# Optimization experiments

Measured on AMD Instinct MI355X. Metric: run time of the kernel, lower is better.

Reference implementation:

```python
import jax, jax.numpy as jnp
import numpy as np

WIN = 7          # window height/width
P = 10           # prompts_len
HEADS = 12
B0 = 32          # image batch (spa_prompts batch)
NW = 64          # windows per image
NW_TOK = WIN * WIN  # 49


def _relative_position_index(w):
    coords = np.stack(np.meshgrid(np.arange(w), np.arange(w), indexing='ij'))  # [2,w,w]
    flat = coords.reshape(2, -1)                        # [2, w*w]
    rel = flat[:, :, None] - flat[:, None, :]           # [2, w*w, w*w]
    rel = rel.transpose(1, 2, 0).astype(np.int64)       # [w*w, w*w, 2]
    rel[..., 0] += w - 1
    rel[..., 1] += w - 1
    rel[..., 0] *= 2 * w - 1
    return rel.sum(-1)                                  # [w*w, w*w]

REL_IDX = jnp.asarray(_relative_position_index(WIN))    # [49,49] int


def setup_inputs() -> dict:
    key = jax.random.key(0)
    ks = jax.random.split(key, 8)
    dim = 384
    return {
        'x': jax.random.normal(ks[0], (B0 * NW, NW_TOK, dim), jnp.float32),
        'spa_prompts': jax.random.normal(ks[1], (B0, P, dim), jnp.float32),
        'mask': jax.random.normal(ks[2], (NW, NW_TOK, NW_TOK), jnp.float32),
        'bias_table': jax.random.normal(ks[3], (169, HEADS), jnp.float32) * 0.02,
        'w_qkv': jax.random.normal(ks[4], (3 * dim, dim), jnp.float32) * 0.02,
        'b_qkv': jax.random.normal(ks[5], (3 * dim,), jnp.float32) * 0.02,
        'w_proj': jax.random.normal(ks[6], (dim, dim), jnp.float32) * 0.02,
        'b_proj': jax.random.normal(ks[7], (dim,), jnp.float32) * 0.02,
    }


def reference(x, spa_prompts, mask, bias_table, w_qkv, b_qkv, w_proj, b_proj):
    B_, Nw, C = x.shape
    b0 = spa_prompts.shape[0]
    nW = B_ // b0
    hd = C // HEADS
    scale = hd ** -0.5

    # broadcast prompts to every window and prepend
    prompts = jnp.broadcast_to(spa_prompts[:, None], (b0, nW, P, C)).reshape(B_, P, C)
    xc = jnp.concatenate([prompts, x], axis=1)          # [B_, N, C], N = P + Nw
    N = xc.shape[1]

    qkv = xc @ w_qkv.T + b_qkv                          # [B_, N, 3C]
    qkv = qkv.reshape(B_, N, 3, HEADS, hd).transpose(2, 0, 3, 1, 4)
    q, k, v = qkv[0], qkv[1], qkv[2]                    # [B_, H, N, hd]

    attn_weight = jnp.einsum('bhnd,bhmd->bhnm', q, k)   # unscaled, returned

    # relative position bias gathered for the window block, padded over prompt rows/cols
    rpb = bias_table[REL_IDX.reshape(-1)].reshape(NW_TOK, NW_TOK, HEADS)
    rpb = rpb.transpose(2, 0, 1)                        # [H, 49, 49]
    bias_full = jnp.pad(rpb, ((0, 0), (P, 0), (P, 0)))  # [H, N, N]

    attn = attn_weight * scale + bias_full[None]

    mask_full = jnp.pad(mask, ((0, 0), (P, 0), (P, 0)))  # [nW, N, N]
    attn = attn.reshape(b0, nW, HEADS, N, N) + mask_full[None, :, None]
    attn = jax.nn.softmax(attn.reshape(B_, HEADS, N, N), axis=-1)

    out = jnp.einsum('bhnm,bhmd->bnhd', attn, v).reshape(B_, N, C)
    out = out @ w_proj.T + b_proj

    prompts_out = out[:, :P].reshape(b0, nW, P, C).mean(axis=1)
    x_out = out[:, P:]
    return (x_out, attn_weight, prompts_out)
```

## Files before the change

kernel.cpp:

```cpp
#include <hip/hip_runtime.h>
#include <hip/hip_bf16.h>

#define P     10
#define NTOK  59
#define HEADS 12
#define NWTOK 49

#define AW_OFF 38535168
#define PO_OFF 124096512

typedef __attribute__((ext_vector_type(8))) short short8;
typedef __attribute__((ext_vector_type(8))) unsigned short ushort8;
typedef __attribute__((ext_vector_type(4))) float floatx4;
typedef float f4u __attribute__((ext_vector_type(4), aligned(4)));
typedef unsigned int uint_g __attribute__((address_space(1)));
typedef unsigned int uint_l __attribute__((address_space(3)));

__device__ __forceinline__ unsigned short f2b(float f) {
  unsigned u = __builtin_bit_cast(unsigned, f);
  u += 0x7fffu + ((u >> 16) & 1u);
  return (unsigned short)(u >> 16);
}

__device__ __forceinline__ void gll16(const void* g, void* l) {
  __builtin_amdgcn_global_load_lds((const uint_g*)g, (uint_l*)l, 16, 0, 0);
}

__device__ __forceinline__ int xcd_swz(int bid, int nwg) {
  const int q = nwg >> 3, r = nwg & 7;
  const int xcd = bid & 7, ord = bid >> 3;
  return (xcd < r ? xcd * (q + 1) : r * (q + 1) + (xcd - r) * q) + ord;
}

__global__ __launch_bounds__(256) void convert_w_kernel(
    const float* __restrict__ w, unsigned short* __restrict__ wb) {
  const int i = (blockIdx.x * 256 + threadIdx.x) * 8;
  const float4 a = *(const float4*)(w + i);
  const float4 b = *(const float4*)(w + i + 4);
  ushort8 o;
  o[0] = f2b(a.x); o[1] = f2b(a.y); o[2] = f2b(a.z); o[3] = f2b(a.w);
  o[4] = f2b(b.x); o[5] = f2b(b.y); o[6] = f2b(b.z); o[7] = f2b(b.w);
  *(ushort8*)(wb + i) = o;
}

__global__ __launch_bounds__(256) void combo_kernel(
    const float* __restrict__ mask, const float* __restrict__ bias_table,
    float* __restrict__ combo) {
  const int bid = blockIdx.x;
  const int h = bid % HEADS, wnd = bid / HEADS;
#pragma unroll
  for (int e0 = 0; e0 < 4096; e0 += 256) {
    const int e = e0 + threadIdx.x;
    const int ti = e >> 6, tj = e & 63;
    float v = 0.f;
    if (ti >= P && ti < NTOK && tj >= P && tj < NTOK) {
      const int a = ti - P, c = tj - P;
      const int ai = a / 7, aj = a - ai * 7;
      const int bi = c / 7, bj = c - bi * 7;
      const int ridx = (ai - bi + 6) * 13 + (aj - bj + 6);
      v = bias_table[ridx * HEADS + h] + mask[((size_t)wnd * 49 + a) * 49 + c];
    }
    combo[((size_t)bid << 12) + e] = v;
  }
}

__global__ __launch_bounds__(256) void gemm_qkv_kernel(
    const unsigned short* __restrict__ xb, const unsigned short* __restrict__ xp,
    const unsigned short* __restrict__ Bw, const float* __restrict__ b_qkv,
    unsigned short* __restrict__ qkx, unsigned short* __restrict__ qkp) {
  __shared__ unsigned short sbuf[18432];
  unsigned short* Asw = sbuf;
  unsigned short* Bsw = sbuf + 8192;
  const int t = threadIdx.x;
  const int w = t >> 6, lane = t & 63;
  const int lr = lane & 15, lg = lane >> 4;
  const int w0 = w >> 1, w1 = w & 1;
  const int wg = xcd_swz(blockIdx.x, 9 * 787);
  const int cb = wg % 9;
  const int my = wg / 9;
  const bool isP = my >= 784;
  const int n0 = cb * 128;
  const int srow = lane >> 3, cpos = lane & 7;

  floatx4 acc[4][4];
#pragma unroll
  for (int mr = 0; mr < 4; ++mr)
#pragma unroll
    for (int nc = 0; nc < 4; ++nc) acc[mr][nc] = (floatx4)0.f;

  for (int k0 = 0; k0 < 384; k0 += 64) {
#pragma unroll
    for (int i = 0; i < 4; ++i) {
      const int r = (w * 4 + i) * 8 + srow;
      const int c = cpos ^ (r & 7);
      const unsigned short* asrc;
      if (!isP) {
        asrc = xb + (size_t)(my * 128 + r) * 384 + k0 + c * 8;
      } else {
        int mp = (my - 784) * 128 + r;
        if (mp > 319) mp = 319;
        asrc = xp + (size_t)mp * 384 + k0 + c * 8;
      }
      gll16(asrc, Asw + (w * 4 + i) * 512);
      gll16(Bw + (size_t)(n0 + r) * 384 + k0 + c * 8, Bsw + (w * 4 + i) * 512);
    }
    __syncthreads();
#pragma unroll
    for (int kh = 0; kh < 2; ++kh) {
      short8 af[4], bf[4];
#pragma unroll
      for (int mr = 0; mr < 4; ++mr) {
        const int r = w0 * 64 + mr * 16 + lr;
        af[mr] = *(const short8*)(Asw + r * 64 + (((kh * 4 + lg) ^ (r & 7)) * 8));
      }
#pragma unroll
      for (int nc = 0; nc < 4; ++nc) {
        const int r = w1 * 64 + nc * 16 + lr;
        bf[nc] = *(const short8*)(Bsw + r * 64 + (((kh * 4 + lg) ^ (r & 7)) * 8));
      }
#pragma unroll
      for (int mr = 0; mr < 4; ++mr)
#pragma unroll
        for (int nc = 0; nc < 4; ++nc)
          acc[mr][nc] = __builtin_amdgcn_mfma_f32_16x16x32_bf16(
              af[mr], bf[nc], acc[mr][nc], 0, 0, 0);
    }
    __syncthreads();
  }

  const int sec = cb / 3;
  const int nis = (cb - sec * 3) * 128;
  float bias[4];
#pragma unroll
  for (int nc = 0; nc < 4; ++nc)
    bias[nc] = b_qkv[n0 + w1 * 64 + nc * 16 + lr];

  unsigned short* rp = sbuf + w * 4608;
#pragma unroll
  for (int mr = 0; mr < 4; ++mr)
#pragma unroll
    for (int nc = 0; nc < 4; ++nc)
#pragma unroll
      for (int reg = 0; reg < 4; ++reg)
        rp[(mr * 16 + lg * 4 + reg) * 72 + nc * 16 + lr] =
            f2b(acc[mr][nc][reg] + bias[nc]);
  __syncthreads();

  const int rr = lane;
  unsigned short* dst = nullptr;
  if (!isP) {
    const int m = my * 128 + w0 * 64 + rr;
    const int bb = m / 49, tok = m - bb * 49;
    dst = qkx + ((size_t)(bb * 3 + sec) * 49 + tok) * 384 + nis + w1 * 64;
  } else {
    const int mp = (my - 784) * 128 + w0 * 64 + rr;
    if (mp < 320) {
      const int b0 = mp / 10, ptok = mp - b0 * 10;
      dst = qkp + ((size_t)(b0 * 3 + sec) * 10 + ptok) * 384 + nis + w1 * 64;
    }
  }
  if (dst) {
#pragma unroll
    for (int u = 0; u < 8; ++u)
      *(ushort8*)(dst + u * 8) = *(const ushort8*)(rp + rr * 72 + u * 8);
  }
}

__global__ __launch_bounds__(256) void attn_kernel(
    const unsigned short* __restrict__ qkx, const unsigned short* __restrict__ qkp,
    const float* __restrict__ combo, float* __restrict__ aw_out,
    unsigned short* __restrict__ attn_bf) {
  __shared__ char lds[14976];
  unsigned short* qs = (unsigned short*)(lds);
  unsigned short* ks = (unsigned short*)(lds + 5120);
  unsigned short* vt = (unsigned short*)(lds + 10240);
  unsigned short* Pm = (unsigned short*)(lds);

  const int blk = blockIdx.x;
  const int b = blk / HEADS, h = blk - b * HEADS;
  const int t = threadIdx.x;
  const int w = t >> 6, lane = t & 63, lr = lane & 15, lg = lane >> 4;

  if (t < 236) {
    const int row = t >> 2, dc = (t & 3) * 8;
    ushort8 q8, k8, v8;
    if (row < P) {
      const unsigned short* pb =
          qkp + ((size_t)((b >> 6) * 3) * 10 + row) * 384 + h * 32 + dc;
      q8 = *(const ushort8*)(pb);
      k8 = *(const ushort8*)(pb + 10 * 384);
      v8 = *(const ushort8*)(pb + 20 * 384);
    } else {
      const unsigned short* xbp =
          qkx + ((size_t)(b * 3) * 49 + (row - P)) * 384 + h * 32 + dc;
      q8 = *(const ushort8*)(xbp);
      k8 = *(const ushort8*)(xbp + 49 * 384);
      v8 = *(const ushort8*)(xbp + 98 * 384);
    }
    *(ushort8*)(qs + row * 40 + dc) = q8;
    *(ushort8*)(ks + row * 40 + dc) = k8;
#pragma unroll
    for (int j = 0; j < 8; ++j) vt[(dc + j) * 74 + row] = v8[j];
  } else {
    const int e = t - 236;
#pragma unroll
    for (int jj = 0; jj < 8; ++jj) {
      const int f = e * 8 + jj;
      vt[(f / 5) * 74 + 59 + (f % 5)] = 0;
    }
  }
  __syncthreads();

  const int q = w * 16 + lr;
  const short8 qa = *(const short8*)(qs + q * 40 + lg * 8);
  floatx4 sacc[4];
#pragma unroll
  for (int nt = 0; nt < 4; ++nt) {
    const short8 kb = *(const short8*)(ks + (nt * 16 + lr) * 40 + lg * 8);
    sacc[nt] = __builtin_amdgcn_mfma_f32_16x16x32_bf16(kb, qa, (floatx4)0.f, 0, 0, 0);
  }

  if (q < NTOK) {
    float* rowp = aw_out + (size_t)blk * 3481 + q * 59;
#pragma unroll
    for (int nt = 0; nt < 3; ++nt)
      *(f4u*)(rowp + nt * 16 + lg * 4) = __builtin_bit_cast(f4u, sacc[nt]);
    if (lg < 2) {
      *(f4u*)(rowp + 48 + lg * 4) = __builtin_bit_cast(f4u, sacc[3]);
    } else if (lg == 2) {
      rowp[56] = sacc[3][0];
      rowp[57] = sacc[3][1];
      rowp[58] = sacc[3][2];
    }
  }

  const float scale = 0.17677669529663687f;
  const float* comb = combo + (((size_t)((b & 63) * HEADS + h)) << 12) + q * 64;
  float ev[4][4];
  float mx = -3.0e38f;
#pragma unroll
  for (int nt = 0; nt < 4; ++nt) {
    const float4 c4 = *(const float4*)(comb + nt * 16 + lg * 4);
    const float cc[4] = {c4.x, c4.y, c4.z, c4.w};
#pragma unroll
    for (int reg = 0; reg < 4; ++reg) {
      const int kk2 = nt * 16 + lg * 4 + reg;
      const float v = (q < NTOK && kk2 < NTOK)
                          ? fmaf(sacc[nt][reg], scale, cc[reg])
                          : -3.0e38f;
      ev[nt][reg] = v;
      mx = fmaxf(mx, v);
    }
  }
  mx = fmaxf(mx, __shfl_xor(mx, 16));
  mx = fmaxf(mx, __shfl_xor(mx, 32));
  float sm = 0.f;
#pragma unroll
  for (int nt = 0; nt < 4; ++nt)
#pragma unroll
    for (int reg = 0; reg < 4; ++reg) {
      const float e = __expf(ev[nt][reg] - mx);
      ev[nt][reg] = e;
      sm += e;
    }
  sm += __shfl_xor(sm, 16);
  sm += __shfl_xor(sm, 32);
  const float inv = 1.0f / sm;

  __syncthreads();
#pragma unroll
  for (int nt = 0; nt < 4; ++nt) {
    uint2 uu;
    uu.x = (unsigned)f2b(ev[nt][0] * inv) | ((unsigned)f2b(ev[nt][1] * inv) << 16);
    uu.y = (unsigned)f2b(ev[nt][2] * inv) | ((unsigned)f2b(ev[nt][3] * inv) << 16);
    *(uint2*)(Pm + q * 72 + nt * 16 + lg * 4) = uu;
  }

  floatx4 oacc[2];
  oacc[0] = (floatx4)0.f; oacc[1] = (floatx4)0.f;
#pragma unroll
  for (int kk = 0; kk < 2; ++kk) {
    const short8 pa = *(const short8*)(Pm + (w * 16 + lr) * 72 + kk * 32 + lg * 8);
#pragma unroll
    for (int nt = 0; nt < 2; ++nt) {
      const short8 vb = *(const short8*)(vt + (nt * 16 + lr) * 74 + kk * 32 + lg * 8);
      oacc[nt] = __builtin_amdgcn_mfma_f32_16x16x32_bf16(pa, vb, oacc[nt], 0, 0, 0);
    }
  }

  unsigned short* wb = Pm + w * 1152;
#pragma unroll
  for (int nt = 0; nt < 2; ++nt)
#pragma unroll
    for (int reg = 0; reg < 4; ++reg)
      wb[(lg * 4 + reg) * 40 + nt * 16 + lr] = f2b(oacc[nt][reg]);
  const int rr = lane >> 2, c8 = (lane & 3) * 8;
  const int row = w * 16 + rr;
  if (row < NTOK) {
    const ushort8 ov = *(const ushort8*)(wb + rr * 40 + c8);
    *(ushort8*)(attn_bf + ((size_t)(b * NTOK + row)) * 384 + h * 32 + c8) = ov;
  }
}

__global__ __launch_bounds__(256) void gemm_proj_kernel(
    const unsigned short* __restrict__ A, const unsigned short* __restrict__ Bw,
    const float* __restrict__ b_proj, float* __restrict__ x_out,
    float* __restrict__ pbuf) {
  __shared__ unsigned short Asw[8192];
  __shared__ unsigned short Bsw[8192];
  const int t = threadIdx.x;
  const int w = t >> 6, lane = t & 63;
  const int lr = lane & 15, lg = lane >> 4;
  const int w0 = w >> 1, w1 = w & 1;
  const int wg = xcd_swz(blockIdx.x, 3 * 944);
  const size_t m0 = (size_t)(wg / 3) * 128;
  const int n0 = (wg % 3) * 128;
  const int srow = lane >> 3, cpos = lane & 7;

  floatx4 acc[4][4];
#pragma unroll
  for (int mr = 0; mr < 4; ++mr)
#pragma unroll
    for (int nc = 0; nc < 4; ++nc) acc[mr][nc] = (floatx4)0.f;

  for (int k0 = 0; k0 < 384; k0 += 64) {
#pragma unroll
    for (int i = 0; i < 4; ++i) {
      const int r = (w * 4 + i) * 8 + srow;
      const int c = cpos ^ (r & 7);
      gll16(A + (m0 + r) * 384 + k0 + c * 8, Asw + (w * 4 + i) * 512);
      gll16(Bw + (size_t)(n0 + r) * 384 + k0 + c * 8, Bsw + (w * 4 + i) * 512);
    }
    __syncthreads();
#pragma unroll
    for (int kh = 0; kh < 2; ++kh) {
      short8 af[4], bf[4];
#pragma unroll
      for (int mr = 0; mr < 4; ++mr) {
        const int r = w0 * 64 + mr * 16 + lr;
        af[mr] = *(const short8*)(Asw + r * 64 + (((kh * 4 + lg) ^ (r & 7)) * 8));
      }
#pragma unroll
      for (int nc = 0; nc < 4; ++nc) {
        const int r = w1 * 64 + nc * 16 + lr;
        bf[nc] = *(const short8*)(Bsw + r * 64 + (((kh * 4 + lg) ^ (r & 7)) * 8));
      }
#pragma unroll
      for (int mr = 0; mr < 4; ++mr)
#pragma unroll
        for (int nc = 0; nc < 4; ++nc)
          acc[mr][nc] = __builtin_amdgcn_mfma_f32_16x16x32_bf16(
              af[mr], bf[nc], acc[mr][nc], 0, 0, 0);
    }
    __syncthreads();
  }

  float bias[4]; int nn[4];
#pragma unroll
  for (int nc = 0; nc < 4; ++nc) {
    nn[nc] = n0 + w1 * 64 + nc * 16 + lr;
    bias[nc] = b_proj[nn[nc]];
  }
#pragma unroll
  for (int mr = 0; mr < 4; ++mr)
#pragma unroll
    for (int reg = 0; reg < 4; ++reg) {
      const int m = (int)m0 + w0 * 64 + mr * 16 + lg * 4 + reg;
      const int bb = m / 59, tok = m - bb * 59;
      float* dst = (tok >= P)
          ? x_out + (size_t)(bb * NWTOK + tok - P) * 384
          : pbuf + (size_t)(bb * P + tok) * 384;
#pragma unroll
      for (int nc = 0; nc < 4; ++nc)
        dst[nn[nc]] = acc[mr][nc][reg] + bias[nc];
    }
}

__global__ __launch_bounds__(256) void reduce_prompts_kernel(
    const float* __restrict__ pbuf, float* __restrict__ po) {
  const int o = blockIdx.x * 256 + threadIdx.x;
  const int b0 = o / 3840;
  const int rem = o - b0 * 3840;
  const float* base = pbuf + (size_t)b0 * 64 * 3840 + rem;
  float s = 0.f;
#pragma unroll 8
  for (int w = 0; w < 64; ++w) s += base[(size_t)w * 3840];
  po[o] = s * (1.f / 64.f);
}

extern "C" void kernel_launch(void* const* d_in, const int* in_sizes, int n_in,
                              void* d_out, int out_size, void* d_ws, size_t ws_size,
                              hipStream_t stream) {
  const float* x          = (const float*)d_in[0];
  const float* spa        = (const float*)d_in[1];
  const float* mask       = (const float*)d_in[2];
  const float* bias_table = (const float*)d_in[3];
  const float* w_qkv      = (const float*)d_in[4];
  const float* b_qkv      = (const float*)d_in[5];
  const float* w_proj     = (const float*)d_in[6];
  const float* b_proj     = (const float*)d_in[7];
  float* out = (float*)d_out;

  unsigned short* x_bf     = (unsigned short*)d_ws;
  unsigned short* attn_bf  = (unsigned short*)d_ws;
  unsigned short* xp_bf    = (unsigned short*)((char*)d_ws + 77070336ULL);
  unsigned short* wqkv_bf  = (unsigned short*)((char*)d_ws + 77316096ULL);
  unsigned short* qkx      = (unsigned short*)((char*)d_ws + 92798976ULL);
  unsigned short* qkp      = (unsigned short*)((char*)d_ws + 324009984ULL);
  unsigned short* wproj_bf = (unsigned short*)((char*)d_ws + 324747264ULL);
  float*          pbuf     = (float*)((char*)d_ws + 325042176ULL);
  float*          combo    = (float*)((char*)d_ws + 356499456ULL);

  convert_w_kernel<<<18816, 256, 0, stream>>>(x, x_bf);
  convert_w_kernel<<<60, 256, 0, stream>>>(spa, xp_bf);
  convert_w_kernel<<<216, 256, 0, stream>>>(w_qkv, wqkv_bf);
  convert_w_kernel<<<72, 256, 0, stream>>>(w_proj, wproj_bf);
  combo_kernel<<<768, 256, 0, stream>>>(mask, bias_table, combo);
  gemm_qkv_kernel<<<9 * 787, 256, 0, stream>>>(x_bf, xp_bf, wqkv_bf, b_qkv,
                                               qkx, qkp);
  attn_kernel<<<2048 * HEADS, 256, 0, stream>>>(qkx, qkp, combo, out + AW_OFF,
                                                attn_bf);
  gemm_proj_kernel<<<3 * 944, 256, 0, stream>>>(attn_bf, wproj_bf, b_proj,
                                                out, pbuf);
  reduce_prompts_kernel<<<480, 256, 0, stream>>>(pbuf, out + PO_OFF);
}
```

Before: 596.4 us.

## Fuse fp32-to-bf16 conversion of activations into QKV GEMM A-tile loads

Removes the separate conversion kernels for x and the prompts. The QKV GEMM now reads fp32 activations directly, converts them to bf16 in registers and writes them to swizzled LDS, instead of loading a pre-converted bf16 copy through direct global-to-LDS loads. This saves writing and re-reading a large bf16 copy of x. In exchange, each GEMM tile reads twice the bytes and the A loads go through registers, and x is re-read by all 9 column blocks. The attention kernel's block index is also remapped with the XCD swizzle to improve cache locality across dies.

```diff
diff --git a/kernel.cpp b/kernel.cpp
--- a/kernel.cpp
+++ b/kernel.cpp
@@ -65,7 +65,7 @@
 }
 
 __global__ __launch_bounds__(256) void gemm_qkv_kernel(
-    const unsigned short* __restrict__ xb, const unsigned short* __restrict__ xp,
+    const float* __restrict__ x, const float* __restrict__ spa,
     const unsigned short* __restrict__ Bw, const float* __restrict__ b_qkv,
     unsigned short* __restrict__ qkx, unsigned short* __restrict__ qkp) {
   __shared__ unsigned short sbuf[18432];
@@ -89,20 +89,36 @@
     for (int nc = 0; nc < 4; ++nc) acc[mr][nc] = (floatx4)0.f;
 
   for (int k0 = 0; k0 < 384; k0 += 64) {
+    ushort8 av[4];
 #pragma unroll
     for (int i = 0; i < 4; ++i) {
       const int r = (w * 4 + i) * 8 + srow;
       const int c = cpos ^ (r & 7);
-      const unsigned short* asrc;
+      const float* asrc;
       if (!isP) {
-        asrc = xb + (size_t)(my * 128 + r) * 384 + k0 + c * 8;
+        asrc = x + (size_t)(my * 128 + r) * 384 + k0 + c * 8;
       } else {
         int mp = (my - 784) * 128 + r;
         if (mp > 319) mp = 319;
-        asrc = xp + (size_t)mp * 384 + k0 + c * 8;
+        asrc = spa + (size_t)mp * 384 + k0 + c * 8;
       }
-      gll16(asrc, Asw + (w * 4 + i) * 512);
+      const float4 v0 = ((const float4*)asrc)[0];
+      const float4 v1 = ((const float4*)asrc)[1];
+      ushort8 o;
+      o[0] = f2b(v0.x); o[1] = f2b(v0.y); o[2] = f2b(v0.z); o[3] = f2b(v0.w);
+      o[4] = f2b(v1.x); o[5] = f2b(v1.y); o[6] = f2b(v1.z); o[7] = f2b(v1.w);
+      av[i] = o;
+    }
+#pragma unroll
+    for (int i = 0; i < 4; ++i) {
+      const int r = (w * 4 + i) * 8 + srow;
+      const int c = cpos ^ (r & 7);
       gll16(Bw + (size_t)(n0 + r) * 384 + k0 + c * 8, Bsw + (w * 4 + i) * 512);
+    }
+#pragma unroll
+    for (int i = 0; i < 4; ++i) {
+      const int r = (w * 4 + i) * 8 + srow;
+      *(ushort8*)(Asw + r * 64 + cpos * 8) = av[i];
     }
     __syncthreads();
 #pragma unroll
@@ -176,7 +192,7 @@
   unsigned short* vt = (unsigned short*)(lds + 10240);
   unsigned short* Pm = (unsigned short*)(lds);
 
-  const int blk = blockIdx.x;
+  const int blk = xcd_swz(blockIdx.x, 2048 * HEADS);
   const int b = blk / HEADS, h = blk - b * HEADS;
   const int t = threadIdx.x;
   const int w = t >> 6, lane = t & 63, lr = lane & 15, lg = lane >> 4;
@@ -401,9 +417,7 @@
   const float* b_proj     = (const float*)d_in[7];
   float* out = (float*)d_out;
 
-  unsigned short* x_bf     = (unsigned short*)d_ws;
   unsigned short* attn_bf  = (unsigned short*)d_ws;
-  unsigned short* xp_bf    = (unsigned short*)((char*)d_ws + 77070336ULL);
   unsigned short* wqkv_bf  = (unsigned short*)((char*)d_ws + 77316096ULL);
   unsigned short* qkx      = (unsigned short*)((char*)d_ws + 92798976ULL);
   unsigned short* qkp      = (unsigned short*)((char*)d_ws + 324009984ULL);
@@ -411,12 +425,10 @@
   float*          pbuf     = (float*)((char*)d_ws + 325042176ULL);
   float*          combo    = (float*)((char*)d_ws + 356499456ULL);
 
-  convert_w_kernel<<<18816, 256, 0, stream>>>(x, x_bf);
-  convert_w_kernel<<<60, 256, 0, stream>>>(spa, xp_bf);
   convert_w_kernel<<<216, 256, 0, stream>>>(w_qkv, wqkv_bf);
   convert_w_kernel<<<72, 256, 0, stream>>>(w_proj, wproj_bf);
   combo_kernel<<<768, 256, 0, stream>>>(mask, bias_table, combo);
-  gemm_qkv_kernel<<<9 * 787, 256, 0, stream>>>(x_bf, xp_bf, wqkv_bf, b_qkv,
+  gemm_qkv_kernel<<<9 * 787, 256, 0, stream>>>(x, spa, wqkv_bf, b_qkv,
                                                qkx, qkp);
   attn_kernel<<<2048 * HEADS, 256, 0, stream>>>(qkx, qkp, combo, out + AW_OFF,
                                                 attn_bf);
```

New measurement: 605.0 us. About the same (+1.4%).

## Fuse window attention with output projection in one per-window kernel

Applied to the files above, without the earlier changes.

Replaces the per-(window,head) attention kernel and the separate projection GEMM with one kernel per window. It loops over all 12 heads, keeps the bf16 attention output for the window in LDS, then multiplies it by w_proj directly. The P matrix now moves between lanes with shuffles instead of a trip through LDS. This removes the global round trip of the attention intermediate and one launch. In exchange it uses about 73KB of LDS per block, which lowers occupancy, runs only 2048 blocks, and reloads w_proj from L2 for every window.

```diff
diff --git a/kernel.cpp b/kernel.cpp
--- a/kernel.cpp
+++ b/kernel.cpp
@@ -166,214 +166,196 @@
   }
 }
 
-__global__ __launch_bounds__(256) void attn_kernel(
+__global__ __launch_bounds__(256) void attn_proj_kernel(
     const unsigned short* __restrict__ qkx, const unsigned short* __restrict__ qkp,
-    const float* __restrict__ combo, float* __restrict__ aw_out,
-    unsigned short* __restrict__ attn_bf) {
-  __shared__ char lds[14976];
-  unsigned short* qs = (unsigned short*)(lds);
-  unsigned short* ks = (unsigned short*)(lds + 5120);
-  unsigned short* vt = (unsigned short*)(lds + 10240);
-  unsigned short* Pm = (unsigned short*)(lds);
-
-  const int blk = blockIdx.x;
-  const int b = blk / HEADS, h = blk - b * HEADS;
+    const float* __restrict__ combo, const unsigned short* __restrict__ wproj,
+    const float* __restrict__ b_proj, float* __restrict__ aw_out,
+    float* __restrict__ x_out, float* __restrict__ pbuf) {
+  __shared__ char lds[74752];
+  unsigned short* Obuf = (unsigned short*)lds;
+  unsigned short* qs   = (unsigned short*)(lds + 50176);
+  unsigned short* ks   = (unsigned short*)(lds + 55296);
+  unsigned short* vt   = (unsigned short*)(lds + 60416);
+  unsigned short* Bst  = (unsigned short*)(lds + 50176);
+
+  const int b = blockIdx.x;
   const int t = threadIdx.x;
   const int w = t >> 6, lane = t & 63, lr = lane & 15, lg = lane >> 4;
-
-  if (t < 236) {
-    const int row = t >> 2, dc = (t & 3) * 8;
-    ushort8 q8, k8, v8;
-    if (row < P) {
-      const unsigned short* pb =
-          qkp + ((size_t)((b >> 6) * 3) * 10 + row) * 384 + h * 32 + dc;
-      q8 = *(const ushort8*)(pb);
-      k8 = *(const ushort8*)(pb + 10 * 384);
-      v8 = *(const ushort8*)(pb + 20 * 384);
+  const float scale = 0.17677669529663687f;
+  const int q = w * 16 + lr;
+
+  for (int h = 0; h < HEADS; ++h) {
+    __syncthreads();
+    if (t < 236) {
+      const int row = t >> 2, dc = (t & 3) * 8;
+      ushort8 q8, k8, v8;
+      if (row < P) {
+        const unsigned short* pb =
+            qkp + ((size_t)((b >> 6) * 3) * 10 + row) * 384 + h * 32 + dc;
+        q8 = *(const ushort8*)(pb);
+        k8 = *(const ushort8*)(pb + 10 * 384);
+        v8 = *(const ushort8*)(pb + 20 * 384);
+      } else {
+        const unsigned short* xbp =
+            qkx + ((size_t)(b * 3) * 49 + (row - P)) * 384 + h * 32 + dc;
+        q8 = *(const ushort8*)(xbp);
+        k8 = *(const ushort8*)(xbp + 49 * 384);
+        v8 = *(const ushort8*)(xbp + 98 * 384);
+      }
+      *(ushort8*)(qs + row * 40 + dc) = q8;
+      *(ushort8*)(ks + row * 40 + dc) = k8;
+#pragma unroll
+      for (int j = 0; j < 8; ++j) vt[(dc + j) * 74 + row] = v8[j];
     } else {
-      const unsigned short* xbp =
-          qkx + ((size_t)(b * 3) * 49 + (row - P)) * 384 + h * 32 + dc;
-      q8 = *(const ushort8*)(xbp);
-      k8 = *(const ushort8*)(xbp + 49 * 384);
-      v8 = *(const ushort8*)(xbp + 98 * 384);
-    }
-    *(ushort8*)(qs + row * 40 + dc) = q8;
-    *(ushort8*)(ks + row * 40 + dc) = k8;
-#pragma unroll
-    for (int j = 0; j < 8; ++j) vt[(dc + j) * 74 + row] = v8[j];
-  } else {
-    const int e = t - 236;
-#pragma unroll
-    for (int jj = 0; jj < 8; ++jj) {
-      const int f = e * 8 + jj;
-      vt[(f / 5) * 74 + 59 + (f % 5)] = 0;
-    }
+      const int e = t - 236;
+#pragma unroll
+      for (int jj = 0; jj < 8; ++jj) {
+        const int f = e * 8 + jj;
+        vt[(f / 5) * 74 + 59 + (f % 5)] = 0;
+      }
+    }
+    __syncthreads();
+
+    const short8 qa = *(const short8*)(qs + q * 40 + lg * 8);
+    floatx4 sacc[4];
+#pragma unroll
+    for (int nt = 0; nt < 4; ++nt) {
+      const short8 kb = *(const short8*)(ks + (nt * 16 + lr) * 40 + lg * 8);
+      sacc[nt] =
+          __builtin_amdgcn_mfma_f32_16x16x32_bf16(kb, qa, (floatx4)0.f, 0, 0, 0);
+    }
+
+    if (q < NTOK) {
+      float* rowp = aw_out + ((size_t)(b * HEADS + h)) * 3481 + q * 59;
+#pragma unroll
+      for (int nt = 0; nt < 3; ++nt)
+        *(f4u*)(rowp + nt * 16 + lg * 4) = __builtin_bit_cast(f4u, sacc[nt]);
+      if (lg < 2) {
+        *(f4u*)(rowp + 48 + lg * 4) = __builtin_bit_cast(f4u, sacc[3]);
+      } else if (lg == 2) {
+        rowp[56] = sacc[3][0]; rowp[57] = sacc[3][1]; rowp[58] = sacc[3][2];
+      }
+    }
+
+    const float* comb =
+        combo + (((size_t)((b & 63) * HEADS + h)) << 12) + q * 64;
+    float ev[4][4];
+    float mx = -3.0e38f;
+#pragma unroll
+    for (int nt = 0; nt < 4; ++nt) {
+      const float4 c4 = *(const float4*)(comb + nt * 16 + lg * 4);
+      const float cc[4] = {c4.x, c4.y, c4.z, c4.w};
+#pragma unroll
+      for (int reg = 0; reg < 4; ++reg) {
+        const int kk2 = nt * 16 + lg * 4 + reg;
+        const float v = (q < NTOK && kk2 < NTOK)
+                            ? fmaf(sacc[nt][reg], scale, cc[reg])
+                            : -3.0e38f;
+        ev[nt][reg] = v;
+        mx = fmaxf(mx, v);
+      }
+    }
+    mx = fmaxf(mx, __shfl_xor(mx, 16));
+    mx = fmaxf(mx, __shfl_xor(mx, 32));
+    float sm = 0.f;
+#pragma unroll
+    for (int nt = 0; nt < 4; ++nt)
+#pragma unroll
+      for (int reg = 0; reg < 4; ++reg) {
+        const float e = __expf(ev[nt][reg] - mx);
+        ev[nt][reg] = e;
+        sm += e;
+      }
+    sm += __shfl_xor(sm, 16);
+    sm += __shfl_xor(sm, 32);
+    const float inv = 1.0f / sm;
+
+    unsigned pk[4][2];
+#pragma unroll
+    for (int nt = 0; nt < 4; ++nt)
+#pragma unroll
+      for (int pp = 0; pp < 2; ++pp)
+        pk[nt][pp] = (unsigned)f2b(ev[nt][2 * pp] * inv) |
+                     ((unsigned)f2b(ev[nt][2 * pp + 1] * inv) << 16);
+
+    floatx4 oacc[2];
+    oacc[0] = (floatx4)0.f; oacc[1] = (floatx4)0.f;
+#pragma unroll
+    for (int kk = 0; kk < 2; ++kk) {
+      unsigned W4[4];
+#pragma unroll
+      for (int jp = 0; jp < 4; ++jp) {
+        const int srcl = lr + 16 * (2 * (lg & 1) + (jp >> 1));
+        const int lo = __shfl((int)pk[2 * kk][jp & 1], srcl);
+        const int hi = __shfl((int)pk[2 * kk + 1][jp & 1], srcl);
+        W4[jp] = (lg >> 1) ? (unsigned)hi : (unsigned)lo;
+      }
+      uint4 wu; wu.x = W4[0]; wu.y = W4[1]; wu.z = W4[2]; wu.w = W4[3];
+      const short8 pa = __builtin_bit_cast(short8, wu);
+#pragma unroll
+      for (int nt = 0; nt < 2; ++nt) {
+        const short8 vb =
+            *(const short8*)(vt + (nt * 16 + lr) * 74 + kk * 32 + lg * 8);
+        oacc[nt] =
+            __builtin_amdgcn_mfma_f32_16x16x32_bf16(pa, vb, oacc[nt], 0, 0, 0);
+      }
+    }
+
+#pragma unroll
+    for (int nt = 0; nt < 2; ++nt)
+#pragma unroll
+      for (int reg = 0; reg < 4; ++reg)
+        Obuf[(w * 16 + lg * 4 + reg) * 392 + h * 32 + nt * 16 + lr] =
+            f2b(oacc[nt][reg]);
   }
   __syncthreads();
 
-  const int q = w * 16 + lr;
-  const short8 qa = *(const short8*)(qs + q * 40 + lg * 8);
-  floatx4 sacc[4];
-#pragma unroll
-  for (int nt = 0; nt < 4; ++nt) {
-    const short8 kb = *(const short8*)(ks + (nt * 16 + lr) * 40 + lg * 8);
-    sacc[nt] = __builtin_amdgcn_mfma_f32_16x16x32_bf16(kb, qa, (floatx4)0.f, 0, 0, 0);
-  }
-
-  if (q < NTOK) {
-    float* rowp = aw_out + (size_t)blk * 3481 + q * 59;
-#pragma unroll
-    for (int nt = 0; nt < 3; ++nt)
-      *(f4u*)(rowp + nt * 16 + lg * 4) = __builtin_bit_cast(f4u, sacc[nt]);
-    if (lg < 2) {
-      *(f4u*)(rowp + 48 + lg * 4) = __builtin_bit_cast(f4u, sacc[3]);
-    } else if (lg == 2) {
-      rowp[56] = sacc[3][0];
-      rowp[57] = sacc[3][1];
-      rowp[58] = sacc[3][2];
-    }
-  }
-
-  const float scale = 0.17677669529663687f;
-  const float* comb = combo + (((size_t)((b & 63) * HEADS + h)) << 12) + q * 64;
-  float ev[4][4];
-  float mx = -3.0e38f;
-#pragma unroll
-  for (int nt = 0; nt < 4; ++nt) {
-    const float4 c4 = *(const float4*)(comb + nt * 16 + lg * 4);
-    const float cc[4] = {c4.x, c4.y, c4.z, c4.w};
-#pragma unroll
-    for (int reg = 0; reg < 4; ++reg) {
-      const int kk2 = nt * 16 + lg * 4 + reg;
-      const float v = (q < NTOK && kk2 < NTOK)
-                          ? fmaf(sacc[nt][reg], scale, cc[reg])
-                          : -3.0e38f;
-      ev[nt][reg] = v;
-      mx = fmaxf(mx, v);
-    }
-  }
-  mx = fmaxf(mx, __shfl_xor(mx, 16));
-  mx = fmaxf(mx, __shfl_xor(mx, 32));
-  float sm = 0.f;
-#pragma unroll
-  for (int nt = 0; nt < 4; ++nt)
-#pragma unroll
-    for (int reg = 0; reg < 4; ++reg) {
-      const float e = __expf(ev[nt][reg] - mx);
-      ev[nt][reg] = e;
-      sm += e;
-    }
-  sm += __shfl_xor(sm, 16);
-  sm += __shfl_xor(sm, 32);
-  const float inv = 1.0f / sm;
-
-  __syncthreads();
-#pragma unroll
-  for (int nt = 0; nt < 4; ++nt) {
-    uint2 uu;
-    uu.x = (unsigned)f2b(ev[nt][0] * inv) | ((unsigned)f2b(ev[nt][1] * inv) << 16);
-    uu.y = (unsigned)f2b(ev[nt][2] * inv) | ((unsigned)f2b(ev[nt][3] * inv) << 16);
-    *(uint2*)(Pm + q * 72 + nt * 16 + lg * 4) = uu;
-  }
-
-  floatx4 oacc[2];
-  oacc[0] = (floatx4)0.f; oacc[1] = (floatx4)0.f;
-#pragma unroll
-  for (int kk = 0; kk < 2; ++kk) {
-    const short8 pa = *(const short8*)(Pm + (w * 16 + lr) * 72 + kk * 32 + lg * 8);
-#pragma unroll
-    for (int nt = 0; nt < 2; ++nt) {
-      const short8 vb = *(const short8*)(vt + (nt * 16 + lr) * 74 + kk * 32 + lg * 8);
-      oacc[nt] = __builtin_amdgcn_mfma_f32_16x16x32_bf16(pa, vb, oacc[nt], 0, 0, 0);
-    }
-  }
-
-  unsigned short* wb = Pm + w * 1152;
-#pragma unroll
-  for (int nt = 0; nt < 2; ++nt)
-#pragma unroll
-    for (int reg = 0; reg < 4; ++reg)
-      wb[(lg * 4 + reg) * 40 + nt * 16 + lr] = f2b(oacc[nt][reg]);
-  const int rr = lane >> 2, c8 = (lane & 3) * 8;
-  const int row = w * 16 + rr;
-  if (row < NTOK) {
-    const ushort8 ov = *(const ushort8*)(wb + rr * 40 + c8);
-    *(ushort8*)(attn_bf + ((size_t)(b * NTOK + row)) * 384 + h * 32 + c8) = ov;
-  }
-}
-
-__global__ __launch_bounds__(256) void gemm_proj_kernel(
-    const unsigned short* __restrict__ A, const unsigned short* __restrict__ Bw,
-    const float* __restrict__ b_proj, float* __restrict__ x_out,
-    float* __restrict__ pbuf) {
-  __shared__ unsigned short Asw[8192];
-  __shared__ unsigned short Bsw[8192];
-  const int t = threadIdx.x;
-  const int w = t >> 6, lane = t & 63;
-  const int lr = lane & 15, lg = lane >> 4;
-  const int w0 = w >> 1, w1 = w & 1;
-  const int wg = xcd_swz(blockIdx.x, 3 * 944);
-  const size_t m0 = (size_t)(wg / 3) * 128;
-  const int n0 = (wg % 3) * 128;
-  const int srow = lane >> 3, cpos = lane & 7;
-
-  floatx4 acc[4][4];
-#pragma unroll
-  for (int mr = 0; mr < 4; ++mr)
-#pragma unroll
-    for (int nc = 0; nc < 4; ++nc) acc[mr][nc] = (floatx4)0.f;
-
-  for (int k0 = 0; k0 < 384; k0 += 64) {
-#pragma unroll
-    for (int i = 0; i < 4; ++i) {
-      const int r = (w * 4 + i) * 8 + srow;
-      const int c = cpos ^ (r & 7);
-      gll16(A + (m0 + r) * 384 + k0 + c * 8, Asw + (w * 4 + i) * 512);
-      gll16(Bw + (size_t)(n0 + r) * 384 + k0 + c * 8, Bsw + (w * 4 + i) * 512);
-    }
-    __syncthreads();
-#pragma unroll
-    for (int kh = 0; kh < 2; ++kh) {
-      short8 af[4], bf[4];
-#pragma unroll
-      for (int mr = 0; mr < 4; ++mr) {
-        const int r = w0 * 64 + mr * 16 + lr;
-        af[mr] = *(const short8*)(Asw + r * 64 + (((kh * 4 + lg) ^ (r & 7)) * 8));
-      }
-#pragma unroll
-      for (int nc = 0; nc < 4; ++nc) {
-        const int r = w1 * 64 + nc * 16 + lr;
-        bf[nc] = *(const short8*)(Bsw + r * 64 + (((kh * 4 + lg) ^ (r & 7)) * 8));
-      }
-#pragma unroll
-      for (int mr = 0; mr < 4; ++mr)
-#pragma unroll
-        for (int nc = 0; nc < 4; ++nc)
-          acc[mr][nc] = __builtin_amdgcn_mfma_f32_16x16x32_bf16(
-              af[mr], bf[nc], acc[mr][nc], 0, 0, 0);
-    }
-    __syncthreads();
-  }
-
-  float bias[4]; int nn[4];
-#pragma unroll
-  for (int nc = 0; nc < 4; ++nc) {
-    nn[nc] = n0 + w1 * 64 + nc * 16 + lr;
-    bias[nc] = b_proj[nn[nc]];
-  }
-#pragma unroll
-  for (int mr = 0; mr < 4; ++mr)
-#pragma unroll
-    for (int reg = 0; reg < 4; ++reg) {
-      const int m = (int)m0 + w0 * 64 + mr * 16 + lg * 4 + reg;
-      const int bb = m / 59, tok = m - bb * 59;
-      float* dst = (tok >= P)
-          ? x_out + (size_t)(bb * NWTOK + tok - P) * 384
-          : pbuf + (size_t)(bb * P + tok) * 384;
-#pragma unroll
-      for (int nc = 0; nc < 4; ++nc)
-        dst[nn[nc]] = acc[mr][nc][reg] + bias[nc];
-    }
+  floatx4 pacc[12];
+#pragma unroll
+  for (int nh = 0; nh < 2; ++nh) {
+#pragma unroll
+    for (int i = 0; i < 12; ++i) pacc[i] = (floatx4)0.f;
+    for (int kch = 0; kch < 6; ++kch) {
+      __syncthreads();
+#pragma unroll
+      for (int i = 0; i < 6; ++i) {
+        const int g = w * 6 + i;
+        const int r = g * 8 + (lane >> 3);
+        const int c = (lane & 7) ^ (r & 7);
+        gll16(wproj + (size_t)(nh * 192 + r) * 384 + kch * 64 + c * 8,
+              Bst + g * 512);
+      }
+      __syncthreads();
+#pragma unroll
+      for (int kh = 0; kh < 2; ++kh) {
+        const short8 af = *(const short8*)(Obuf + (w * 16 + lr) * 392 +
+                                           kch * 64 + kh * 32 + lg * 8);
+#pragma unroll
+        for (int nc = 0; nc < 12; ++nc) {
+          const int nr = nc * 16 + lr;
+          const short8 bf =
+              *(const short8*)(Bst + nr * 64 + (((kh * 4 + lg) ^ (nr & 7)) * 8));
+          pacc[nc] =
+              __builtin_amdgcn_mfma_f32_16x16x32_bf16(af, bf, pacc[nc], 0, 0, 0);
+        }
+      }
+    }
+#pragma unroll
+    for (int nc = 0; nc < 12; ++nc) {
+      const int n = nh * 192 + nc * 16 + lr;
+      const float bias = b_proj[n];
+#pragma unroll
+      for (int reg = 0; reg < 4; ++reg) {
+        const int row = w * 16 + lg * 4 + reg;
+        if (row < NTOK) {
+          float* dst = (row >= P)
+              ? x_out + ((size_t)(b * NWTOK + row - P)) * 384 + n
+              : pbuf + ((size_t)(b * P + row)) * 384 + n;
+          *dst = pacc[nc][reg] + bias;
+        }
+      }
+    }
+  }
 }
 
 __global__ __launch_bounds__(256) void reduce_prompts_kernel(
@@ -402,7 +384,6 @@
   float* out = (float*)d_out;
 
   unsigned short* x_bf     = (unsigned short*)d_ws;
-  unsigned short* attn_bf  = (unsigned short*)d_ws;
   unsigned short* xp_bf    = (unsigned short*)((char*)d_ws + 77070336ULL);
   unsigned short* wqkv_bf  = (unsigned short*)((char*)d_ws + 77316096ULL);
   unsigned short* qkx      = (unsigned short*)((char*)d_ws + 92798976ULL);
@@ -418,9 +399,7 @@
   combo_kernel<<<768, 256, 0, stream>>>(mask, bias_table, combo);
   gemm_qkv_kernel<<<9 * 787, 256, 0, stream>>>(x_bf, xp_bf, wqkv_bf, b_qkv,
                                                qkx, qkp);
-  attn_kernel<<<2048 * HEADS, 256, 0, stream>>>(qkx, qkp, combo, out + AW_OFF,
-                                                attn_bf);
-  gemm_proj_kernel<<<3 * 944, 256, 0, stream>>>(attn_bf, wproj_bf, b_proj,
-                                                out, pbuf);
+  attn_proj_kernel<<<2048, 256, 0, stream>>>(qkx, qkp, combo, wproj_bf, b_proj,
+                                             out + AW_OFF, out, pbuf);
   reduce_prompts_kernel<<<480, 256, 0, stream>>>(pbuf, out + PO_OFF);
 }
```

Result: no change. 597.3 us (+0.1%).
